# Kernel optimization log

Hardware: AMD Instinct MI355X
Metric: run time of the kernel (lower is better)

## Reference

```python
import jax, jax.numpy as jnp
import numpy as np

B, IN, J, K = 1024, 512, 64, 8
CLAMP_MAX = 10.0

def setup_inputs() -> dict:
    key = jax.random.key(0)
    k1, k2 = jax.random.split(key)
    x = jax.random.normal(k1, (B, IN), dtype=jnp.float32)
    T = jax.random.normal(k2, (IN, J, K), dtype=jnp.float32)
    return {"x": x, "T": T}

def reference(x, T):
    # M: [B, J, K]
    M = jnp.einsum('bi,ijk->bjk', x, T)
    # pairwise diff over batch: [B, B, J, K] (matches torch broadcast M1-M2)
    diff = M[None, :, :, :] - M[:, None, :, :]
    sq = jnp.sum(diff * diff, axis=3)          # [B, B, J]
    # safe sqrt (grad 0 at 0, matching torch.norm subgradient on diagonal)
    sq_safe = jnp.where(sq > 0, sq, 1.0)
    norm = jnp.where(sq > 0, jnp.sqrt(sq_safe), 0.0)
    c = jnp.exp(-jnp.minimum(norm, CLAMP_MAX))  # clamp(max=10) then exp(-.)
    feats = jnp.sum(c, axis=1)                  # [B, J]
    return jnp.concatenate([x, feats], axis=1)  # [B, IN + J]
```

## Files before the change

### kernel.cpp

```cpp
#include <hip/hip_runtime.h>

constexpr int NB  = 1024;
constexpr int NIN = 512;
constexpr int NJ  = 64;
constexpr int NK  = 8;
constexpr int NC  = NJ * NK;
constexpr int OUTC = NIN + NJ;
constexpr float EXPN10 = 4.5399929762484854e-05f;
constexpr float FEAT_BASE = 1024.0f * EXPN10;

typedef __bf16 bf16x8 __attribute__((ext_vector_type(8)));
typedef float floatx16 __attribute__((ext_vector_type(16)));

__device__ __forceinline__ unsigned f2bf(float f) {
  unsigned u = __float_as_uint(f);
  u += 0x7FFFu + ((u >> 16) & 1u);
  return u >> 16;
}

__global__ __launch_bounds__(256) void gemm_fused(const float* __restrict__ x,
                                                  const float* __restrict__ T,
                                                  float* __restrict__ Mp,
                                                  uint4* __restrict__ Mb,
                                                  float* __restrict__ na,
                                                  float* __restrict__ out) {
  __shared__ __align__(16) ushort smem_u[2 * 64 * 136];
  ushort* Xs = smem_u;
  ushort* Ts = smem_u + 64 * 136;
  float*  Cs = (float*)smem_u;

  const int tid = threadIdx.x;
  const int b0 = blockIdx.x * 64;
  const int c0 = blockIdx.y * 64;

  const int lane = tid & 63;
  const int w    = tid >> 6;
  const int l31  = lane & 31;
  const int half = lane >> 5;
  const int arow = (w & 1) * 32 + l31;
  const int bcol = (w >> 1) * 32 + l31;

  const int xrow = tid >> 4;
  const int xseg = tid & 15;
  const int pr   = tid >> 4;
  const int coff = (tid & 15) * 4;
  (void)xrow; (void)xseg;

  float4 avA[8], bvA[8], avB[8], bvB[8];

  auto load_slice = [&](int z, float4 (&av)[8], float4 (&bv)[8]) {
#pragma unroll
    for (int t = 0; t < 4; ++t) {
      const int u = t * 256 + tid;
      const int row = u >> 4, seg = u & 15;
      const size_t base = (size_t)(b0 + row) * NIN + z * 128 + seg * 8;
      av[2 * t]     = *(const float4*)&x[base];
      av[2 * t + 1] = *(const float4*)&x[base + 4];
    }
#pragma unroll
    for (int it = 0; it < 4; ++it) {
      const int k0 = it * 32 + pr * 2;
      const size_t base = (size_t)(z * 128 + k0) * NC + c0 + coff;
      bv[2 * it]     = *(const float4*)&T[base];
      bv[2 * it + 1] = *(const float4*)&T[base + NC];
    }
  };

  auto stage_slice = [&](const float4 (&av)[8], const float4 (&bv)[8]) {
#pragma unroll
    for (int t = 0; t < 4; ++t) {
      const int u = t * 256 + tid;
      const int row = u >> 4, seg = u & 15;
      uint4 p;
      p.x = f2bf(av[2 * t].x) | (f2bf(av[2 * t].y) << 16);
      p.y = f2bf(av[2 * t].z) | (f2bf(av[2 * t].w) << 16);
      p.z = f2bf(av[2 * t + 1].x) | (f2bf(av[2 * t + 1].y) << 16);
      p.w = f2bf(av[2 * t + 1].z) | (f2bf(av[2 * t + 1].w) << 16);
      *(uint4*)&Xs[row * 136 + seg * 8] = p;
    }
    unsigned* Tw = (unsigned*)Ts;
#pragma unroll
    for (int it = 0; it < 4; ++it) {
      const float* lo = &bv[2 * it].x;
      const float* hi = &bv[2 * it + 1].x;
#pragma unroll
      for (int q = 0; q < 4; ++q) {
        const unsigned val = f2bf(lo[q]) | (f2bf(hi[q]) << 16);
        Tw[(coff + q) * 68 + it * 16 + pr] = val;
      }
    }
  };

  floatx16 acc = {};
  auto mfma_tile = [&]() {
#pragma unroll
    for (int s = 0; s < 8; ++s) {
      const bf16x8 af = *(const bf16x8*)&Xs[arow * 136 + s * 16 + half * 8];
      const bf16x8 bf = *(const bf16x8*)&Ts[bcol * 136 + s * 16 + half * 8];
      acc = __builtin_amdgcn_mfma_f32_32x32x16_bf16(af, bf, acc, 0, 0, 0);
    }
  };

  load_slice(0, avA, bvA);

  const int bidf = blockIdx.y * 16 + blockIdx.x;
#pragma unroll
  for (int it = 0; it < 5; ++it) {
    const int li = it * 256 + tid;
    if (li < 1152) {
      const int gi = bidf * 1152 + li;
      const int b = gi / (OUTC / 4);
      const int r = gi - b * (OUTC / 4);
      float4 v;
      if (r < NIN / 4) v = ((const float4*)x)[b * (NIN / 4) + r];
      else v = float4{FEAT_BASE, FEAT_BASE, FEAT_BASE, FEAT_BASE};
      ((float4*)out)[gi] = v;
    }
  }

  load_slice(1, avB, bvB);
  stage_slice(avA, bvA);
  __syncthreads();
  mfma_tile();
  __syncthreads();
  load_slice(2, avA, bvA);
  stage_slice(avB, bvB);
  __syncthreads();
  mfma_tile();
  __syncthreads();
  load_slice(3, avB, bvB);
  stage_slice(avA, bvA);
  __syncthreads();
  mfma_tile();
  __syncthreads();
  stage_slice(avB, bvB);
  __syncthreads();
  mfma_tile();
  __syncthreads();

#pragma unroll
  for (int reg = 0; reg < 16; ++reg) {
    const int row = (reg & 3) + 8 * (reg >> 2) + 4 * half;
    Cs[((w & 1) * 32 + row) * 68 + (w >> 1) * 32 + l31] = acc[reg];
  }
  __syncthreads();

#pragma unroll
  for (int pass = 0; pass < 2; ++pass) {
    const int jl = (tid >> 6) + pass * 4;
    const int b  = tid & 63;
    const float4 m0 = *(const float4*)&Cs[b * 68 + jl * 8];
    const float4 m1 = *(const float4*)&Cs[b * 68 + jl * 8 + 4];
    const int j_g = blockIdx.y * 8 + jl;
    const int idx = j_g * NB + b0 + b;
    ((float4*)Mp)[idx * 2]     = m0;
    ((float4*)Mp)[idx * 2 + 1] = m1;
    float s = m0.x * m0.x;
    s = fmaf(m0.y, m0.y, s); s = fmaf(m0.z, m0.z, s); s = fmaf(m0.w, m0.w, s);
    s = fmaf(m1.x, m1.x, s); s = fmaf(m1.y, m1.y, s); s = fmaf(m1.z, m1.z, s);
    s = fmaf(m1.w, m1.w, s);
    na[idx] = s;
    uint4 pk;
    pk.x = f2bf(m0.x) | (f2bf(m0.y) << 16);
    pk.y = f2bf(m0.z) | (f2bf(m0.w) << 16);
    pk.z = f2bf(m1.x) | (f2bf(m1.y) << 16);
    pk.w = f2bf(m1.z) | (f2bf(m1.w) << 16);
    Mb[idx] = pk;
  }
}

__global__ __launch_bounds__(256) void pairwise_kernel(const uint4* __restrict__ Mb,
                                                       const float* __restrict__ na,
                                                       const float* __restrict__ Mp,
                                                       float* __restrict__ out) {
  const int j    = blockIdx.x;
  const int ag   = blockIdx.y;
  const int bh   = blockIdx.z;
  const int tid  = threadIdx.x;
  const int lane = tid & 63;
  const int w    = tid >> 6;
  const int col  = lane & 31;
  const int h    = lane >> 5;
  const int jb   = j * NB;

  __shared__ uint4 Mb_s[513];
  __shared__ float nb_s[512];
  __shared__ float na_s[128];

  const int bbeg = bh * 512;
  Mb_s[tid]       = Mb[jb + bbeg + tid];
  Mb_s[tid + 256] = Mb[jb + bbeg + tid + 256];
  nb_s[tid]       = na[jb + bbeg + tid];
  nb_s[tid + 256] = na[jb + bbeg + tid + 256];
  if (tid == 0) Mb_s[512] = uint4{0u, 0u, 0u, 0u};

  const int a0 = ag * 128 + w * 32;
  if (lane < 32) na_s[w * 32 + lane] = na[jb + a0 + lane];

  uint4 araw = uint4{0u, 0u, 0u, 0u};
  if (lane < 32) araw = Mb[jb + a0 + lane];
  const bf16x8 af = __builtin_bit_cast(bf16x8, araw);

  __syncthreads();

  float c995[16];
#pragma unroll
  for (int reg = 0; reg < 16; ++reg) {
    const int row = (reg & 3) + 8 * (reg >> 2) + 4 * h;
    c995[reg] = 0.995f * na_s[w * 32 + row];
  }

  const floatx16 zero = {};

#pragma unroll 2
  for (int bt = 0; bt < 16; ++bt) {
    const int bidx = bt * 32 + col;
    const uint4 braw = Mb_s[lane < 32 ? bidx : 512];
    const bf16x8 bf = __builtin_bit_cast(bf16x8, braw);
    const floatx16 P = __builtin_amdgcn_mfma_f32_32x32x16_bf16(af, bf, zero, 0, 0, 0);
    const float nb_l = nb_s[bidx];
    const float rhs = 100.0f - 0.995f * nb_l;

    float t = fmaf(-2.0f, P[0], c995[0]);
#pragma unroll
    for (int reg = 1; reg < 16; ++reg)
      t = fminf(t, fmaf(-2.0f, P[reg], c995[reg]));

    if (__any(t < rhs)) {
#pragma unroll
      for (int reg = 0; reg < 16; ++reg) {
        if (fmaf(-2.0f, P[reg], c995[reg]) < rhs) {
          const int row = (reg & 3) + 8 * (reg >> 2) + 4 * h;
          const int a = a0 + row;
          const int b = bbeg + bt * 32 + col;
          float corr;
          if (a == b) {
            corr = 1.0f - EXPN10;
          } else {
            const float4 av0 = ((const float4*)Mp)[(jb + a) * 2];
            const float4 av1 = ((const float4*)Mp)[(jb + a) * 2 + 1];
            const float4 bv0 = ((const float4*)Mp)[(jb + b) * 2];
            const float4 bv1 = ((const float4*)Mp)[(jb + b) * 2 + 1];
            float d = av0.x - bv0.x; float sq = d * d;
            d = av0.y - bv0.y; sq = fmaf(d, d, sq);
            d = av0.z - bv0.z; sq = fmaf(d, d, sq);
            d = av0.w - bv0.w; sq = fmaf(d, d, sq);
            d = av1.x - bv1.x; sq = fmaf(d, d, sq);
            d = av1.y - bv1.y; sq = fmaf(d, d, sq);
            d = av1.z - bv1.z; sq = fmaf(d, d, sq);
            d = av1.w - bv1.w; sq = fmaf(d, d, sq);
            const float nrm = sqrtf(sq);
            corr = (nrm < 10.0f) ? (__expf(-nrm) - EXPN10) : 0.0f;
          }
          if (corr != 0.0f) atomicAdd(&out[a * OUTC + NIN + j], corr);
        }
      }
    }
  }
}

extern "C" void kernel_launch(void* const* d_in, const int* in_sizes, int n_in,
                              void* d_out, int out_size, void* d_ws, size_t ws_size,
                              hipStream_t stream) {
  const float* x = (const float*)d_in[0];
  const float* T = (const float*)d_in[1];
  float* out = (float*)d_out;

  float* Mp  = (float*)d_ws;
  float* na  = Mp + (size_t)NJ * NB * NK;
  uint4* Mb  = (uint4*)(na + (size_t)NJ * NB);

  gemm_fused<<<dim3(16, 8), 256, 0, stream>>>(x, T, Mp, Mb, na, out);
  pairwise_kernel<<<dim3(NJ, 8, 2), 256, 0, stream>>>(Mb, na, Mp, out);
}
```

Measured before the change: 74.25 us.

## Prefetch all GEMM K-slices upfront and read pairwise operands directly from global

The GEMM kernel now issues global loads for all four K-slices into registers before the output-copy loop, rather than double-buffering them. This exposes more memory-level parallelism at the cost of many more live registers, which may lower occupancy. The pairwise kernel drops its shared-memory staging and __syncthreads, reading Mb and norms from global (through cache) inside the loop, and raises unrolling to 4. That removes the LDS fill and barrier latency but leaves the loop dependent on global or L2 latency.

```diff
diff --git a/kernel.cpp b/kernel.cpp
--- a/kernel.cpp
+++ b/kernel.cpp
@@ -40,13 +40,10 @@
   const int arow = (w & 1) * 32 + l31;
   const int bcol = (w >> 1) * 32 + l31;
 
-  const int xrow = tid >> 4;
-  const int xseg = tid & 15;
   const int pr   = tid >> 4;
   const int coff = (tid & 15) * 4;
-  (void)xrow; (void)xseg;
-
-  float4 avA[8], bvA[8], avB[8], bvB[8];
+
+  float4 av0[8], bv0[8], av1[8], bv1[8], av2[8], bv2[8], av3[8], bv3[8];
 
   auto load_slice = [&](int z, float4 (&av)[8], float4 (&bv)[8]) {
 #pragma unroll
@@ -101,7 +98,11 @@
     }
   };
 
-  load_slice(0, avA, bvA);
+  load_slice(0, av0, bv0);
+  load_slice(1, av1, bv1);
+  load_slice(2, av2, bv2);
+  load_slice(3, av3, bv3);
+  __builtin_amdgcn_sched_barrier(0);
 
   const int bidf = blockIdx.y * 16 + blockIdx.x;
 #pragma unroll
@@ -118,22 +119,19 @@
     }
   }
 
-  load_slice(1, avB, bvB);
-  stage_slice(avA, bvA);
-  __syncthreads();
-  mfma_tile();
-  __syncthreads();
-  load_slice(2, avA, bvA);
-  stage_slice(avB, bvB);
-  __syncthreads();
-  mfma_tile();
-  __syncthreads();
-  load_slice(3, avB, bvB);
-  stage_slice(avA, bvA);
-  __syncthreads();
-  mfma_tile();
-  __syncthreads();
-  stage_slice(avB, bvB);
+  stage_slice(av0, bv0);
+  __syncthreads();
+  mfma_tile();
+  __syncthreads();
+  stage_slice(av1, bv1);
+  __syncthreads();
+  mfma_tile();
+  __syncthreads();
+  stage_slice(av2, bv2);
+  __syncthreads();
+  mfma_tile();
+  __syncthreads();
+  stage_slice(av3, bv3);
   __syncthreads();
   mfma_tile();
   __syncthreads();
@@ -183,42 +181,30 @@
   const int h    = lane >> 5;
   const int jb   = j * NB;
 
-  __shared__ uint4 Mb_s[513];
-  __shared__ float nb_s[512];
-  __shared__ float na_s[128];
-
   const int bbeg = bh * 512;
-  Mb_s[tid]       = Mb[jb + bbeg + tid];
-  Mb_s[tid + 256] = Mb[jb + bbeg + tid + 256];
-  nb_s[tid]       = na[jb + bbeg + tid];
-  nb_s[tid + 256] = na[jb + bbeg + tid + 256];
-  if (tid == 0) Mb_s[512] = uint4{0u, 0u, 0u, 0u};
-
   const int a0 = ag * 128 + w * 32;
-  if (lane < 32) na_s[w * 32 + lane] = na[jb + a0 + lane];
 
   uint4 araw = uint4{0u, 0u, 0u, 0u};
   if (lane < 32) araw = Mb[jb + a0 + lane];
   const bf16x8 af = __builtin_bit_cast(bf16x8, araw);
 
-  __syncthreads();
-
   float c995[16];
 #pragma unroll
   for (int reg = 0; reg < 16; ++reg) {
     const int row = (reg & 3) + 8 * (reg >> 2) + 4 * h;
-    c995[reg] = 0.995f * na_s[w * 32 + row];
+    c995[reg] = 0.995f * na[jb + a0 + row];
   }
 
   const floatx16 zero = {};
-
-#pragma unroll 2
+  const uint4 zed = uint4{0u, 0u, 0u, 0u};
+
+#pragma unroll 4
   for (int bt = 0; bt < 16; ++bt) {
     const int bidx = bt * 32 + col;
-    const uint4 braw = Mb_s[lane < 32 ? bidx : 512];
+    const uint4 braw = (lane < 32) ? Mb[jb + bbeg + bidx] : zed;
     const bf16x8 bf = __builtin_bit_cast(bf16x8, braw);
+    const float nb_l = na[jb + bbeg + bidx];
     const floatx16 P = __builtin_amdgcn_mfma_f32_32x32x16_bf16(af, bf, zero, 0, 0, 0);
-    const float nb_l = nb_s[bidx];
     const float rhs = 100.0f - 0.995f * nb_l;
 
     float t = fmaf(-2.0f, P[0], c995[0]);
```

Result: slower. 81.72 us (+10.1%).
